# Kernel tuning notes

Measured on AMD Instinct MI355X. Metric: run time of the kernel, lower is better.

The kernel has to match this reference:

```python
import jax, jax.numpy as jnp
import numpy as np

N1 = 8192; N2 = 8192; E = 131072
D_IN = 128; H = 256; T = 32; B = 16
GCN_DIMS = [(D_IN, H), (H, H), (H, H)]


def _gcn_conv(x, edge_index, W):
    # PyG GCNConv (bias=False): add self-loops, symmetric D^-1/2 (A+I) D^-1/2 normalization.
    n = x.shape[0]
    h = x @ W
    loop = jnp.arange(n, dtype=edge_index.dtype)
    src = jnp.concatenate([edge_index[0], loop])
    dst = jnp.concatenate([edge_index[1], loop])
    deg = jax.ops.segment_sum(jnp.ones(dst.shape[0], h.dtype), dst, num_segments=n)
    dinv = jnp.where(deg > 0, jax.lax.rsqrt(deg), 0.0)
    norm = dinv[src] * dinv[dst]
    return jax.ops.segment_sum(norm[:, None] * h[src], dst, num_segments=n)


def _layer(f1, f2, ei1, ei2, Wg, Wu, bu, last):
    c1 = _gcn_conv(f1, ei1, Wg)
    c2 = _gcn_conv(f2, ei2, Wg)
    sim = f1 @ f2.T                      # [N1, N2] 'dot' similarity
    a1 = jax.nn.softmax(sim, axis=1)     # row softmax
    a2 = jax.nn.softmax(sim, axis=0)     # col softmax
    att1 = a1 @ f2                       # [N1, d]
    att2 = a2.T @ f1                     # [N2, d]
    g1 = jnp.concatenate([c1, f1, f1 - att1], axis=1) @ Wu + bu
    g2 = jnp.concatenate([c2, f2, f2 - att2], axis=1) @ Wu + bu
    if last:
        return g1, g2                    # last layer: no tanh, no dropout
    return jnp.tanh(g1), jnp.tanh(g2)    # dropout is a no-op in eval mode


def _forward(f1, f2, ei1, ei2, avg_v, gcn_Ws, upd_Ws, upd_bs,
             gated_W, gated_b, tn_W, tn_Wb, tn_b, fc1_W, fc1_b, sc_W, sc_b):
    n_layers = len(gcn_Ws)
    for i in range(n_layers):
        f1, f2 = _layer(f1, f2, ei1, ei2, gcn_Ws[i], upd_Ws[i], upd_bs[i],
                        last=(i == n_layers - 1))
    # gated readout: sum(sigmoid(gated(x)) * x)
    p1 = jnp.sum(jax.nn.sigmoid(f1 @ gated_W + gated_b) * f1, axis=0)  # [H]
    p2 = jnp.sum(jax.nn.sigmoid(f2 @ gated_W + gated_b) * f2, axis=0)  # [H]
    # NTN (TensorNetworkModule)
    scoring = jnp.einsum('i,ijt,j->t', p1, tn_W, p2)                   # bilinear term [T]
    block = tn_Wb @ jnp.concatenate([p1, p2])                          # [T]
    ntn = jax.nn.relu(scoring + block + tn_b)
    s = jnp.tanh(ntn @ fc1_W + fc1_b)                                  # [B]
    score = jax.nn.sigmoid(s @ sc_W + sc_b)                            # [1]
    pre_ged = -jnp.log(score) * avg_v                                  # target_mode='exp'
    return score.reshape(-1), pre_ged.reshape(-1)


def setup_inputs():
    key = jax.random.key(0)
    ks = jax.random.split(key, 32)
    rn = lambda k, sh, s=0.05: jax.random.normal(k, sh, dtype=jnp.float32) * s
    inp = {
        'features_1': jax.random.normal(ks[0], (N1, D_IN), dtype=jnp.float32),
        'features_2': jax.random.normal(ks[1], (N2, D_IN), dtype=jnp.float32),
        'edge_index_1': jax.random.randint(ks[2], (2, E), 0, N1, dtype=jnp.int32),
        'edge_index_2': jax.random.randint(ks[3], (2, E), 0, N2, dtype=jnp.int32),
        'avg_v': jnp.full((1,), 12.0, dtype=jnp.float32),
    }
    for i, (di, do) in enumerate(GCN_DIMS):
        inp[f'gcn_W{i}'] = rn(ks[4 + i], (di, do))
        inp[f'upd_W{i}'] = rn(ks[8 + i], (2 * di + do, do))
        inp[f'upd_b{i}'] = jnp.zeros((do,), jnp.float32)
    inp['gated_W'] = rn(ks[12], (H, H)); inp['gated_b'] = jnp.zeros((H,), jnp.float32)
    inp['tn_W'] = rn(ks[13], (H, H, T))
    inp['tn_Wb'] = rn(ks[14], (T, 2 * H)); inp['tn_b'] = jnp.zeros((T,), jnp.float32)
    inp['fc1_W'] = rn(ks[15], (T, B)); inp['fc1_b'] = jnp.zeros((B,), jnp.float32)
    inp['sc_W'] = rn(ks[16], (B, 1)); inp['sc_b'] = jnp.zeros((1,), jnp.float32)
    return inp


def reference(features_1, features_2, edge_index_1, edge_index_2, avg_v,
              gcn_W0, gcn_W1, gcn_W2, upd_W0, upd_W1, upd_W2,
              upd_b0, upd_b1, upd_b2, gated_W, gated_b,
              tn_W, tn_Wb, tn_b, fc1_W, fc1_b, sc_W, sc_b):
    return _forward(features_1, features_2, edge_index_1, edge_index_2, avg_v,
                    [gcn_W0, gcn_W1, gcn_W2], [upd_W0, upd_W1, upd_W2],
                    [upd_b0, upd_b1, upd_b2], gated_W, gated_b,
                    tn_W, tn_Wb, tn_b, fc1_W, fc1_b, sc_W, sc_b)
```

## Files before the change

kernel.cpp:

```cpp
#include <hip/hip_runtime.h>
#include <hip/hip_bf16.h>
#include <stdint.h>

#define NN 8192
#define EDG 131072
#define NSPLIT 4

typedef __attribute__((ext_vector_type(8))) short bf16x8;
typedef __attribute__((ext_vector_type(4))) float f32x4;
typedef unsigned short us;

__device__ __forceinline__ us f2bf(float f) {
  union { float f; unsigned u; } v; v.f = f;
  return (us)((v.u + 0x7fffu + ((v.u >> 16) & 1u)) >> 16);
}

__device__ __forceinline__ us f2bf_trunc(float f) {
  union { float f; unsigned u; } v; v.f = f;
  return (us)(v.u >> 16);
}

__device__ __forceinline__ float bf2f(us u) {
  union { unsigned u; float f; } v; v.u = ((unsigned)u) << 16;
  return v.f;
}

__device__ __forceinline__ void load_lds16(const void* g, void* l) {
  __builtin_amdgcn_global_load_lds(
      (__attribute__((address_space(1))) void*)(uintptr_t)g,
      (__attribute__((address_space(3))) void*)(uintptr_t)l,
      16, 0, 0);
}

template <int EPI>
__global__ __launch_bounds__(256) void gemm_k(
    const us* __restrict__ A, int lda, const us* __restrict__ Bt, int ldb,
    const float* __restrict__ bias, void* __restrict__ Cv, int ldc, int K) {
  __shared__ alignas(16) us As[64 * 32];
  __shared__ alignas(16) us Bs[128 * 32];
  const int t = threadIdx.x;
  const int wave = t >> 6, lane = t & 63;
  const int wrow = wave * 16;
  const int lrow = lane & 15, quad = lane >> 4;
  const int rowBase = blockIdx.x * 64;
  const int colBase = blockIdx.y * 128;
  const int sr = t >> 2, sch = t & 3;

  f32x4 acc[8];
#pragma unroll
  for (int j = 0; j < 8; j++) acc[j] = f32x4{0.f, 0.f, 0.f, 0.f};

  for (int kb = 0; kb < K; kb += 32) {
    __syncthreads();
    const us* asrc = A + (size_t)(rowBase + sr) * lda + kb + sch * 8;
    load_lds16(asrc, (char*)As + t * 16);
    const us* bsrc = Bt + (size_t)(colBase + sr) * ldb + kb + sch * 8;
    load_lds16(bsrc, (char*)Bs + t * 16);
    load_lds16(bsrc + (size_t)64 * ldb, (char*)Bs + t * 16 + 4096);
    __syncthreads();
    bf16x8 af = *(const bf16x8*)&As[(wrow + lrow) * 32 + quad * 8];
#pragma unroll
    for (int j = 0; j < 8; j++) {
      bf16x8 bfr = *(const bf16x8*)&Bs[(j * 16 + lrow) * 32 + quad * 8];
      acc[j] = __builtin_amdgcn_mfma_f32_16x16x32_bf16(af, bfr, acc[j], 0, 0, 0);
    }
  }

#pragma unroll
  for (int j = 0; j < 8; j++) {
    int col = colBase + j * 16 + lrow;
#pragma unroll
    for (int r = 0; r < 4; r++) {
      int row = rowBase + wrow + quad * 4 + r;
      size_t idx = (size_t)row * ldc + col;
      float v = acc[j][r];
      if (EPI == 0) ((float*)Cv)[idx] = v;
      else if (EPI == 2) ((float*)Cv)[idx] = v + bias[col];
      else if (EPI == 4) ((us*)Cv)[idx] = f2bf(v + bias[col]);
      else if (EPI == 5) ((us*)Cv)[idx] = f2bf(tanhf(v + bias[col]));
      else ((us*)Cv)[idx] = f2bf(v * bias[row]);
    }
  }
}

template <int DIN>
__global__ __launch_bounds__(256, 2) void flash_att(
    const us* __restrict__ Q, const us* __restrict__ K,
    const us* __restrict__ Vt, us* __restrict__ Opart,
    float* __restrict__ mpart, float* __restrict__ lpart, int kvPerSplit) {
  constexpr int NKC = DIN / 32;
  constexpr int OJ = DIN / 16;
  __shared__ alignas(16) us As[2][64 * 32];
  __shared__ alignas(16) us KB[2][256 * 32];
  __shared__ alignas(16) us Vs[2][DIN * 32];
  us* Ps = &KB[0][0];

  const int t = threadIdx.x;
  const int wave = t >> 6, lane = t & 63;
  const int wrow = wave * 16;
  const int lrow = lane & 15, quad = lane >> 4;
  const int rowBase = blockIdx.x * 64;
  const int split = blockIdx.y;
  const int kv0 = split * kvPerSplit;
  const int sr = t >> 2, sch = t & 3;
  const int pkey = ((lrow >> 2) ^ lrow) & 3;

  auto stageQ = [&](int kc, int buf) {
    const us* qsrc = Q + (size_t)(rowBase + sr) * DIN + kc * 32 + sch * 8;
    load_lds16(qsrc, (char*)&As[buf][0] + t * 16);
  };
  auto stageK = [&](int kt, int kc, int buf) {
    const us* ksrc = K + (size_t)(kt + sr) * DIN + kc * 32 + sch * 8;
#pragma unroll
    for (int p = 0; p < 4; p++)
      load_lds16(ksrc + (size_t)(p * 64) * DIN, (char*)&KB[buf][0] + p * 4096 + t * 16);
  };
  auto stageV = [&](int kt, int cc, int buf) {
#pragma unroll
    for (int p = 0; p < DIN / 64; p++) {
      const us* vsrc = Vt + (size_t)(p * 64 + sr) * NN + kt + cc * 32 + sch * 8;
      load_lds16(vsrc, (char*)&Vs[buf][0] + p * 4096 + t * 16);
    }
  };

  stageQ(0, 0);
  stageV(kv0, 0, 0);

  float m_i[4], l_i[4];
#pragma unroll
  for (int r = 0; r < 4; r++) { m_i[r] = -3.0e38f; l_i[r] = 0.f; }
  f32x4 accO[OJ];
#pragma unroll
  for (int j = 0; j < OJ; j++) accO[j] = f32x4{0.f, 0.f, 0.f, 0.f};

  for (int kt = kv0; kt < kv0 + kvPerSplit; kt += 256) {
    __syncthreads();
    stageK(kt, 0, 0);

    f32x4 accS[16];
#pragma unroll
    for (int j = 0; j < 16; j++) accS[j] = f32x4{0.f, 0.f, 0.f, 0.f};
    for (int kc = 0; kc < NKC; kc++) {
      const int buf = kc & 1;
      __syncthreads();
      if (kc + 1 < NKC) { stageK(kt, kc + 1, buf ^ 1); stageQ(kc + 1, buf ^ 1); }
      bf16x8 af = *(const bf16x8*)&As[buf][(wrow + lrow) * 32 + quad * 8];
#pragma unroll
      for (int j = 0; j < 16; j++) {
        bf16x8 bfr = *(const bf16x8*)&KB[buf][(j * 16 + lrow) * 32 + quad * 8];
        accS[j] = __builtin_amdgcn_mfma_f32_16x16x32_bf16(af, bfr, accS[j], 0, 0, 0);
      }
    }

    float alpha[4];
#pragma unroll
    for (int r = 0; r < 4; r++) {
      float v = accS[0][r];
#pragma unroll
      for (int j = 1; j < 16; j++) v = fmaxf(v, accS[j][r]);
#pragma unroll
      for (int mask = 1; mask < 16; mask <<= 1) v = fmaxf(v, __shfl_xor(v, mask));
      float mn = fmaxf(m_i[r], v);
      alpha[r] = __expf(m_i[r] - mn);
      m_i[r] = mn;
    }
    __syncthreads();
    float ts[4] = {0.f, 0.f, 0.f, 0.f};
#pragma unroll
    for (int j = 0; j < 16; j++)
#pragma unroll
      for (int r = 0; r < 4; r++) {
        float p = __expf(accS[j][r] - m_i[r]);
        ts[r] += p;
        int prow = wrow + quad * 4 + r;
        int key = (quad ^ r) & 3;
        int g = 2 * j + (lrow >> 3);
        Ps[prow * 256 + ((g ^ (key << 1)) << 3) + (lrow & 7)] = f2bf_trunc(p);
      }
#pragma unroll
    for (int r = 0; r < 4; r++) {
      float v = ts[r];
#pragma unroll
      for (int mask = 1; mask < 16; mask <<= 1) v += __shfl_xor(v, mask);
      l_i[r] = l_i[r] * alpha[r] + v;
    }
#pragma unroll
    for (int j = 0; j < OJ; j++)
#pragma unroll
      for (int r = 0; r < 4; r++) accO[j][r] *= alpha[r];

    const bool hasNext = (kt + 256 < kv0 + kvPerSplit);
    for (int cc = 0; cc < 8; cc++) {
      if (cc) __syncthreads();
      if (cc + 1 < 8) stageV(kt, cc + 1, (cc + 1) & 1);
      else if (hasNext) { stageV(kt + 256, 0, 0); stageQ(0, 0); }
      const int gk = cc * 4 + quad;
      bf16x8 af = *(const bf16x8*)&Ps[(wrow + lrow) * 256 + ((gk ^ (pkey << 1)) << 3)];
      const us* vb = &Vs[cc & 1][0];
#pragma unroll
      for (int j = 0; j < OJ; j++) {
        bf16x8 bfr = *(const bf16x8*)&vb[(j * 16 + lrow) * 32 + quad * 8];
        accO[j] = __builtin_amdgcn_mfma_f32_16x16x32_bf16(af, bfr, accO[j], 0, 0, 0);
      }
    }
  }

#pragma unroll
  for (int j = 0; j < OJ; j++)
#pragma unroll
    for (int r = 0; r < 4; r++) {
      int row = rowBase + wrow + quad * 4 + r;
      int col = j * 16 + lrow;
      Opart[((size_t)split * NN + row) * DIN + col] = f2bf(accO[j][r]);
    }
  if (lrow == 0) {
#pragma unroll
    for (int r = 0; r < 4; r++) {
      int row = rowBase + wrow + quad * 4 + r;
      mpart[(size_t)split * NN + row] = m_i[r];
      lpart[(size_t)split * NN + row] = l_i[r];
    }
  }
}

__global__ void merge_cat(const us* __restrict__ Op, const float* __restrict__ mp,
                          const float* __restrict__ lp, const us* __restrict__ cbuf,
                          const us* __restrict__ fbf, us* __restrict__ cat,
                          int din, int W) {
  int i = blockIdx.y;
  int c = blockIdx.x * 256 + threadIdx.x;
  us o;
  if (c < 256) {
    o = cbuf[(size_t)i * 256 + c];
  } else if (c < 256 + din) {
    o = fbf[(size_t)i * din + (c - 256)];
  } else {
    int f = c - 256 - din;
    float m[NSPLIT], w[NSPLIT];
    float M = -3.0e38f;
#pragma unroll
    for (int s = 0; s < NSPLIT; s++) { m[s] = mp[(size_t)s * NN + i]; M = fmaxf(M, m[s]); }
    float L = 0.f;
#pragma unroll
    for (int s = 0; s < NSPLIT; s++) { w[s] = __expf(m[s] - M); L += lp[(size_t)s * NN + i] * w[s]; }
    float a = 0.f;
#pragma unroll
    for (int s = 0; s < NSPLIT; s++)
      a += w[s] * bf2f(Op[((size_t)s * NN + i) * din + f]);
    o = f2bf(bf2f(fbf[(size_t)i * din + f]) - a / L);
  }
  cat[(size_t)i * W + c] = o;
}


__global__ void ws_sentinel(float* out) { out[0] = 12345.0f; out[1] = 12345.0f; }

__global__ void cvt_bf16(const float* __restrict__ in, us* __restrict__ out, int n) {
  int i = (blockIdx.x * 256 + threadIdx.x) * 4;
  if (i < n) {
    f32x4 v = *(const f32x4*)(in + i);
    uint2 p;
    p.x = f2bf(v.x) | ((unsigned)f2bf(v.y) << 16);
    p.y = f2bf(v.z) | ((unsigned)f2bf(v.w) << 16);
    *(uint2*)(out + i) = p;
  }
}

__global__ void transpose_bf16(const float* __restrict__ src, us* __restrict__ dst,
                               int R, int C) {
  __shared__ float tile[32][33];
  int c0 = blockIdx.x * 32, r0 = blockIdx.y * 32;
  int x = threadIdx.x, y = threadIdx.y;
  for (int i = y; i < 32; i += 8) tile[i][x] = src[(size_t)(r0 + i) * C + c0 + x];
  __syncthreads();
  for (int i = y; i < 32; i += 8) dst[(size_t)(c0 + i) * R + r0 + x] = f2bf(tile[x][i]);
}

__global__ void transpose_bb(const us* __restrict__ src, us* __restrict__ dst,
                             int R, int C) {
  __shared__ us tile[32][33];
  int c0 = blockIdx.x * 32, r0 = blockIdx.y * 32;
  int x = threadIdx.x, y = threadIdx.y;
  for (int i = y; i < 32; i += 8) tile[i][x] = src[(size_t)(r0 + i) * C + c0 + x];
  __syncthreads();
  for (int i = y; i < 32; i += 8) dst[(size_t)(c0 + i) * R + r0 + x] = tile[x][i];
}

__global__ void deg_count(const int* __restrict__ dst, int* __restrict__ deg) {
  int e = blockIdx.x * 256 + threadIdx.x;
  atomicAdd(&deg[dst[e]], 1);
}

__global__ void make_dinv(const int* __restrict__ deg, float* __restrict__ dinv) {
  int v = blockIdx.x * 256 + threadIdx.x;
  dinv[v] = rsqrtf((float)(deg[v] + 1));
}

__global__ void scan_deg(const int* __restrict__ deg, int* __restrict__ rowstart) {
  __shared__ int part[1024];
  int t = threadIdx.x;
  int base = t * 8;
  int local[8];
  int s = 0;
#pragma unroll
  for (int i = 0; i < 8; i++) { local[i] = s; s += deg[base + i]; }
  part[t] = s;
  __syncthreads();
  for (int off = 1; off < 1024; off <<= 1) {
    int v = (t >= off) ? part[t - off] : 0;
    __syncthreads();
    part[t] += v;
    __syncthreads();
  }
  int offset = (t == 0) ? 0 : part[t - 1];
#pragma unroll
  for (int i = 0; i < 8; i++) rowstart[base + i] = offset + local[i];
  if (t == 1023) rowstart[8192] = offset + s;
}

__global__ void csr_fill(const int* __restrict__ src, const int* __restrict__ dst,
                         int* __restrict__ cursor, int* __restrict__ csr_src) {
  int e = blockIdx.x * 256 + threadIdx.x;
  int pos = atomicAdd(&cursor[dst[e]], 1);
  csr_src[pos] = src[e];
}

__global__ __launch_bounds__(256) void gcn_agg_b(
    const int* __restrict__ rowstart, const int* __restrict__ csr_src,
    const float* __restrict__ dinv, const us* __restrict__ hs,
    us* __restrict__ c) {
  int node = blockIdx.x * 4 + (threadIdx.x >> 6);
  int lane = threadIdx.x & 63;
  const us* hp = hs + lane * 4;
  uint2 u = *(const uint2*)(hp + (size_t)node * 256);
  float a0 = bf2f(u.x & 0xffffu), a1 = bf2f(u.x >> 16);
  float a2 = bf2f(u.y & 0xffffu), a3 = bf2f(u.y >> 16);
  int s0 = rowstart[node], s1 = rowstart[node + 1];
  for (int j = s0; j < s1; j++) {
    int s = csr_src[j];
    uint2 v = *(const uint2*)(hp + (size_t)s * 256);
    a0 += bf2f(v.x & 0xffffu); a1 += bf2f(v.x >> 16);
    a2 += bf2f(v.y & 0xffffu); a3 += bf2f(v.y >> 16);
  }
  float dn = dinv[node];
  uint2 o;
  o.x = f2bf(a0 * dn) | ((unsigned)f2bf(a1 * dn) << 16);
  o.y = f2bf(a2 * dn) | ((unsigned)f2bf(a3 * dn) << 16);
  *(uint2*)(c + (size_t)node * 256 + lane * 4) = o;
}

__global__ void gated_pool(const float* __restrict__ q, const us* __restrict__ f,
                           float* __restrict__ p) {
  int col = threadIdx.x;
  int r0 = blockIdx.x * 128;
  float a = 0.f;
  for (int i = r0; i < r0 + 128; i++) {
    float qv = q[(size_t)i * 256 + col];
    a += bf2f(f[(size_t)i * 256 + col]) / (1.f + __expf(-qv));
  }
  atomicAdd(&p[col], a);
}

__global__ void ntn_bilinear(const float* __restrict__ p1, const float* __restrict__ tnW,
                             float* __restrict__ tmp) {
  int c = blockIdx.x * 256 + threadIdx.x;
  float a = 0.f;
#pragma unroll 8
  for (int i = 0; i < 256; i++) a += p1[i] * tnW[(size_t)i * 8192 + c];
  tmp[c] = a;
}

__global__ void ntn_final(const float* __restrict__ tmp, const float* __restrict__ p1,
                          const float* __restrict__ p2, const float* __restrict__ tnWb,
                          const float* __restrict__ tnb, const float* __restrict__ fc1W,
                          const float* __restrict__ fc1b, const float* __restrict__ scW,
                          const float* __restrict__ scb, const float* __restrict__ avgv,
                          float* __restrict__ out) {
  __shared__ float pc[512];
  __shared__ float ntn[32];
  __shared__ float sarr[16];
  int t = threadIdx.x;
  pc[t] = p1[t];
  pc[256 + t] = p2[t];
  __syncthreads();
  if (t < 32) {
    float sc = 0.f;
    for (int j = 0; j < 256; j++) sc += tmp[j * 32 + t] * pc[256 + j];
    float bl = 0.f;
    for (int k = 0; k < 512; k++) bl += tnWb[t * 512 + k] * pc[k];
    float v = sc + bl + tnb[t];
    ntn[t] = v > 0.f ? v : 0.f;
  }
  __syncthreads();
  if (t < 16) {
    float a = fc1b[t];
    for (int i = 0; i < 32; i++) a += ntn[i] * fc1W[i * 16 + t];
    sarr[t] = tanhf(a);
  }
  __syncthreads();
  if (t == 0) {
    float a = scb[0];
    for (int b = 0; b < 16; b++) a += sarr[b] * scW[b];
    float score = 1.f / (1.f + expf(-a));
    out[0] = score;
    out[1] = -logf(score) * avgv[0];
  }
}


extern "C" void kernel_launch(void* const* d_in, const int* in_sizes, int n_in,
                              void* d_out, int out_size, void* d_ws, size_t ws_size,
                              hipStream_t stream) {
  (void)in_sizes; (void)n_in; (void)out_size;
  const float* feat1 = (const float*)d_in[0];
  const float* feat2 = (const float*)d_in[1];
  const int* ei1 = (const int*)d_in[2];
  const int* ei2 = (const int*)d_in[3];
  const float* avgv = (const float*)d_in[4];
  const float* gcnW[3] = {(const float*)d_in[5], (const float*)d_in[8], (const float*)d_in[11]};
  const float* updW[3] = {(const float*)d_in[6], (const float*)d_in[9], (const float*)d_in[12]};
  const float* updb[3] = {(const float*)d_in[7], (const float*)d_in[10], (const float*)d_in[13]};
  const float* gatedW = (const float*)d_in[14];
  const float* gatedb = (const float*)d_in[15];
  const float* tnW = (const float*)d_in[16];
  const float* tnWb = (const float*)d_in[17];
  const float* tnb = (const float*)d_in[18];
  const float* fc1W = (const float*)d_in[19];
  const float* fc1b = (const float*)d_in[20];
  const float* scW = (const float*)d_in[21];
  const float* scb = (const float*)d_in[22];
  float* out = (float*)d_out;

  char* wp = (char*)d_ws;
  auto take = [&](size_t b) { char* p = wp; wp += (b + 255) & ~(size_t)255; return p; };
  us* Op = (us*)take((size_t)NSPLIT * NN * 256 * 2);
  us* cat1 = (us*)take((size_t)NN * 768 * 2);
  us* cat2 = (us*)take((size_t)NN * 768 * 2);
  us* fA1 = (us*)take((size_t)NN * 256 * 2);
  us* fA2 = (us*)take((size_t)NN * 256 * 2);
  us* fB1 = (us*)take((size_t)NN * 256 * 2);
  us* fB2 = (us*)take((size_t)NN * 256 * 2);
  us* f1bT = (us*)take((size_t)NN * 256 * 2);
  us* f2bT = (us*)take((size_t)NN * 256 * 2);
  us* hs1 = (us*)take((size_t)NN * 256 * 2);
  us* hs2 = (us*)take((size_t)NN * 256 * 2);
  us* cb1 = (us*)take((size_t)NN * 256 * 2);
  us* cb2 = (us*)take((size_t)NN * 256 * 2);
  float* q1 = (float*)take((size_t)NN * 256 * 4);
  float* q2 = (float*)take((size_t)NN * 256 * 4);
  us* WgT[3], *WuT[3];
  for (int l = 0; l < 3; l++) WgT[l] = (us*)take(256 * 256 * 2);
  for (int l = 0; l < 3; l++) WuT[l] = (us*)take(256 * 768 * 2);
  us* gWT = (us*)take(256 * 256 * 2);
  int* deg1 = (int*)take(NN * 4);
  int* deg2 = (int*)take(NN * 4);
  float* dinv1 = (float*)take(NN * 4);
  float* dinv2 = (float*)take(NN * 4);
  int* rs1 = (int*)take((NN + 1) * 4);
  int* rs2 = (int*)take((NN + 1) * 4);
  int* cur1 = (int*)take(NN * 4);
  int* cur2 = (int*)take(NN * 4);
  int* csr1 = (int*)take((size_t)EDG * 4);
  int* csr2 = (int*)take((size_t)EDG * 4);
  float* mp = (float*)take((size_t)NSPLIT * NN * 4);
  float* lp = (float*)take((size_t)NSPLIT * NN * 4);
  float* p1 = (float*)take(1024);
  float* p2 = (float*)take(1024);
  float* tmp = (float*)take(NN * 4);

  size_t need = (size_t)(wp - (char*)d_ws);
  if (need > ws_size) {
    ws_sentinel<<<1, 1, 0, stream>>>(out);
    return;
  }

  hipMemsetAsync(deg1, 0, NN * 4, stream);
  hipMemsetAsync(deg2, 0, NN * 4, stream);
  deg_count<<<EDG / 256, 256, 0, stream>>>(ei1 + EDG, deg1);
  deg_count<<<EDG / 256, 256, 0, stream>>>(ei2 + EDG, deg2);
  make_dinv<<<NN / 256, 256, 0, stream>>>(deg1, dinv1);
  make_dinv<<<NN / 256, 256, 0, stream>>>(deg2, dinv2);
  scan_deg<<<1, 1024, 0, stream>>>(deg1, rs1);
  scan_deg<<<1, 1024, 0, stream>>>(deg2, rs2);
  hipMemcpyAsync(cur1, rs1, NN * 4, hipMemcpyDeviceToDevice, stream);
  hipMemcpyAsync(cur2, rs2, NN * 4, hipMemcpyDeviceToDevice, stream);
  csr_fill<<<EDG / 256, 256, 0, stream>>>(ei1, ei1 + EDG, cur1, csr1);
  csr_fill<<<EDG / 256, 256, 0, stream>>>(ei2, ei2 + EDG, cur2, csr2);

  for (int l = 0; l < 3; l++) {
    int din = (l == 0) ? 128 : 256;
    int W = 256 + 2 * din;
    transpose_bf16<<<dim3(8, din / 32), dim3(32, 8), 0, stream>>>(gcnW[l], WgT[l], din, 256);
    transpose_bf16<<<dim3(8, W / 32), dim3(32, 8), 0, stream>>>(updW[l], WuT[l], W, 256);
  }
  transpose_bf16<<<dim3(8, 8), dim3(32, 8), 0, stream>>>(gatedW, gWT, 256, 256);

  us* f1 = fA1; us* f2 = fA2;
  us* fn1 = fB1; us* fn2 = fB2;
  cvt_bf16<<<NN * 128 / 1024, 256, 0, stream>>>(feat1, f1, NN * 128);
  cvt_bf16<<<NN * 128 / 1024, 256, 0, stream>>>(feat2, f2, NN * 128);

  for (int l = 0; l < 3; l++) {
    const int din = (l == 0) ? 128 : 256;
    const int W = 256 + 2 * din;

    if (l == 0) {
      transpose_bf16<<<dim3(din / 32, NN / 32), dim3(32, 8), 0, stream>>>(feat1, f1bT, NN, din);
      transpose_bf16<<<dim3(din / 32, NN / 32), dim3(32, 8), 0, stream>>>(feat2, f2bT, NN, din);
    } else {
      transpose_bb<<<dim3(din / 32, NN / 32), dim3(32, 8), 0, stream>>>(f1, f1bT, NN, din);
      transpose_bb<<<dim3(din / 32, NN / 32), dim3(32, 8), 0, stream>>>(f2, f2bT, NN, din);
    }

    gemm_k<6><<<dim3(128, 2), 256, 0, stream>>>(f1, din, WgT[l], din, dinv1, hs1, 256, din);
    gemm_k<6><<<dim3(128, 2), 256, 0, stream>>>(f2, din, WgT[l], din, dinv2, hs2, 256, din);

    gcn_agg_b<<<NN / 4, 256, 0, stream>>>(rs1, csr1, dinv1, hs1, cb1);
    gcn_agg_b<<<NN / 4, 256, 0, stream>>>(rs2, csr2, dinv2, hs2, cb2);

    if (l == 0) {
      flash_att<128><<<dim3(NN / 64, NSPLIT), 256, 0, stream>>>(f1, f2, f2bT, Op, mp, lp, NN / NSPLIT);
      merge_cat<<<dim3(W / 256, NN), 256, 0, stream>>>(Op, mp, lp, cb1, f1, cat1, din, W);
      flash_att<128><<<dim3(NN / 64, NSPLIT), 256, 0, stream>>>(f2, f1, f1bT, Op, mp, lp, NN / NSPLIT);
      merge_cat<<<dim3(W / 256, NN), 256, 0, stream>>>(Op, mp, lp, cb2, f2, cat2, din, W);
    } else {
      flash_att<256><<<dim3(NN / 64, NSPLIT), 256, 0, stream>>>(f1, f2, f2bT, Op, mp, lp, NN / NSPLIT);
      merge_cat<<<dim3(W / 256, NN), 256, 0, stream>>>(Op, mp, lp, cb1, f1, cat1, din, W);
      flash_att<256><<<dim3(NN / 64, NSPLIT), 256, 0, stream>>>(f2, f1, f1bT, Op, mp, lp, NN / NSPLIT);
      merge_cat<<<dim3(W / 256, NN), 256, 0, stream>>>(Op, mp, lp, cb2, f2, cat2, din, W);
    }

    if (l < 2) {
      gemm_k<5><<<dim3(128, 2), 256, 0, stream>>>(cat1, W, WuT[l], W, updb[l], fn1, 256, W);
      gemm_k<5><<<dim3(128, 2), 256, 0, stream>>>(cat2, W, WuT[l], W, updb[l], fn2, 256, W);
    } else {
      gemm_k<4><<<dim3(128, 2), 256, 0, stream>>>(cat1, W, WuT[l], W, updb[l], fn1, 256, W);
      gemm_k<4><<<dim3(128, 2), 256, 0, stream>>>(cat2, W, WuT[l], W, updb[l], fn2, 256, W);
    }
    us* s;
    s = f1; f1 = fn1; fn1 = s;
    s = f2; f2 = fn2; fn2 = s;
  }

  gemm_k<2><<<dim3(128, 2), 256, 0, stream>>>(f1, 256, gWT, 256, gatedb, q1, 256, 256);
  gemm_k<2><<<dim3(128, 2), 256, 0, stream>>>(f2, 256, gWT, 256, gatedb, q2, 256, 256);
  hipMemsetAsync(p1, 0, 256 * 4, stream);
  hipMemsetAsync(p2, 0, 256 * 4, stream);
  gated_pool<<<64, 256, 0, stream>>>(q1, f1, p1);
  gated_pool<<<64, 256, 0, stream>>>(q2, f2, p2);

  ntn_bilinear<<<32, 256, 0, stream>>>(p1, tnW, tmp);
  ntn_final<<<1, 256, 0, stream>>>(tmp, p1, p2, tnWb, tnb, fc1W, fc1b, scW, scb, avgv, out);
}
```

Baseline: 1.216 ms.

## Use 2x2 wave tiling in flash attention with cross-wave softmax reduction

Reassigns the four waves of the flash attention block from a 4x1 row split to a 2x2 tile split. Each wave now computes 32 rows by half the key columns for QK^T and half the output columns for PV. This lets each B-fragment LDS read feed two MFMAs, cutting LDS traffic per MFMA. In exchange, row max and row sum must be combined across wave pairs through shared memory, which adds an extra barrier and small LDS arrays per KV tile.

Measured after the change: 1.412 ms. +16.1%, slower.

```diff
diff --git a/kernel.cpp b/kernel.cpp
--- a/kernel.cpp
+++ b/kernel.cpp
@@ -89,15 +89,18 @@
     const us* __restrict__ Vt, us* __restrict__ Opart,
     float* __restrict__ mpart, float* __restrict__ lpart, int kvPerSplit) {
   constexpr int NKC = DIN / 32;
-  constexpr int OJ = DIN / 16;
+  constexpr int OJ = DIN / 32;
   __shared__ alignas(16) us As[2][64 * 32];
   __shared__ alignas(16) us KB[2][256 * 32];
   __shared__ alignas(16) us Vs[2][DIN * 32];
+  __shared__ float redM[2][64];
+  __shared__ float redL[2][64];
   us* Ps = &KB[0][0];
 
   const int t = threadIdx.x;
   const int wave = t >> 6, lane = t & 63;
-  const int wrow = wave * 16;
+  const int wr = wave >> 1;
+  const int wc = wave & 1;
   const int lrow = lane & 15, quad = lane >> 4;
   const int rowBase = blockIdx.x * 64;
   const int split = blockIdx.y;
@@ -126,68 +129,115 @@
   stageQ(0, 0);
   stageV(kv0, 0, 0);
 
-  float m_i[4], l_i[4];
-#pragma unroll
-  for (int r = 0; r < 4; r++) { m_i[r] = -3.0e38f; l_i[r] = 0.f; }
-  f32x4 accO[OJ];
-#pragma unroll
-  for (int j = 0; j < OJ; j++) accO[j] = f32x4{0.f, 0.f, 0.f, 0.f};
+  float m_i[8], l_i[8];
+#pragma unroll
+  for (int x = 0; x < 8; x++) { m_i[x] = -3.0e38f; l_i[x] = 0.f; }
+  f32x4 accO[2][OJ];
+#pragma unroll
+  for (int i = 0; i < 2; i++)
+#pragma unroll
+    for (int j = 0; j < OJ; j++) accO[i][j] = f32x4{0.f, 0.f, 0.f, 0.f};
 
   for (int kt = kv0; kt < kv0 + kvPerSplit; kt += 256) {
     __syncthreads();
     stageK(kt, 0, 0);
 
-    f32x4 accS[16];
-#pragma unroll
-    for (int j = 0; j < 16; j++) accS[j] = f32x4{0.f, 0.f, 0.f, 0.f};
+    f32x4 accS[2][8];
+#pragma unroll
+    for (int i = 0; i < 2; i++)
+#pragma unroll
+      for (int j = 0; j < 8; j++) accS[i][j] = f32x4{0.f, 0.f, 0.f, 0.f};
     for (int kc = 0; kc < NKC; kc++) {
       const int buf = kc & 1;
       __syncthreads();
       if (kc + 1 < NKC) { stageK(kt, kc + 1, buf ^ 1); stageQ(kc + 1, buf ^ 1); }
-      bf16x8 af = *(const bf16x8*)&As[buf][(wrow + lrow) * 32 + quad * 8];
-#pragma unroll
-      for (int j = 0; j < 16; j++) {
-        bf16x8 bfr = *(const bf16x8*)&KB[buf][(j * 16 + lrow) * 32 + quad * 8];
-        accS[j] = __builtin_amdgcn_mfma_f32_16x16x32_bf16(af, bfr, accS[j], 0, 0, 0);
+      bf16x8 af[2];
+#pragma unroll
+      for (int i = 0; i < 2; i++)
+        af[i] = *(const bf16x8*)&As[buf][(wr * 32 + i * 16 + lrow) * 32 + quad * 8];
+#pragma unroll
+      for (int j = 0; j < 8; j++) {
+        bf16x8 bfr = *(const bf16x8*)&KB[buf][(wc * 128 + j * 16 + lrow) * 32 + quad * 8];
+#pragma unroll
+        for (int i = 0; i < 2; i++)
+          accS[i][j] = __builtin_amdgcn_mfma_f32_16x16x32_bf16(af[i], bfr, accS[i][j], 0, 0, 0);
       }
     }
 
-    float alpha[4];
-#pragma unroll
-    for (int r = 0; r < 4; r++) {
-      float v = accS[0][r];
-#pragma unroll
-      for (int j = 1; j < 16; j++) v = fmaxf(v, accS[j][r]);
-#pragma unroll
-      for (int mask = 1; mask < 16; mask <<= 1) v = fmaxf(v, __shfl_xor(v, mask));
-      float mn = fmaxf(m_i[r], v);
-      alpha[r] = __expf(m_i[r] - mn);
-      m_i[r] = mn;
+    float tm[8];
+#pragma unroll
+    for (int i = 0; i < 2; i++)
+#pragma unroll
+      for (int r = 0; r < 4; r++) {
+        float v = accS[i][0][r];
+#pragma unroll
+        for (int j = 1; j < 8; j++) v = fmaxf(v, accS[i][j][r]);
+#pragma unroll
+        for (int mask = 1; mask < 16; mask <<= 1) v = fmaxf(v, __shfl_xor(v, mask));
+        tm[i * 4 + r] = v;
+      }
+    if (lrow == 0) {
+#pragma unroll
+      for (int i = 0; i < 2; i++)
+#pragma unroll
+        for (int r = 0; r < 4; r++)
+          redM[wc][wr * 32 + i * 16 + quad * 4 + r] = tm[i * 4 + r];
     }
     __syncthreads();
-    float ts[4] = {0.f, 0.f, 0.f, 0.f};
-#pragma unroll
-    for (int j = 0; j < 16; j++)
+    float alpha[8];
+#pragma unroll
+    for (int i = 0; i < 2; i++)
 #pragma unroll
       for (int r = 0; r < 4; r++) {
-        float p = __expf(accS[j][r] - m_i[r]);
-        ts[r] += p;
-        int prow = wrow + quad * 4 + r;
-        int key = (quad ^ r) & 3;
-        int g = 2 * j + (lrow >> 3);
-        Ps[prow * 256 + ((g ^ (key << 1)) << 3) + (lrow & 7)] = f2bf_trunc(p);
+        int x = i * 4 + r, row = wr * 32 + i * 16 + quad * 4 + r;
+        float mt = fmaxf(redM[0][row], redM[1][row]);
+        float mn = fmaxf(m_i[x], mt);
+        alpha[x] = __expf(m_i[x] - mn);
+        m_i[x] = mn;
       }
-#pragma unroll
-    for (int r = 0; r < 4; r++) {
-      float v = ts[r];
-#pragma unroll
-      for (int mask = 1; mask < 16; mask <<= 1) v += __shfl_xor(v, mask);
-      l_i[r] = l_i[r] * alpha[r] + v;
-    }
-#pragma unroll
-    for (int j = 0; j < OJ; j++)
-#pragma unroll
-      for (int r = 0; r < 4; r++) accO[j][r] *= alpha[r];
+    float ts[8];
+#pragma unroll
+    for (int x = 0; x < 8; x++) ts[x] = 0.f;
+#pragma unroll
+    for (int i = 0; i < 2; i++)
+#pragma unroll
+      for (int j = 0; j < 8; j++)
+#pragma unroll
+        for (int r = 0; r < 4; r++) {
+          int x = i * 4 + r;
+          float p = __expf(accS[i][j][r] - m_i[x]);
+          ts[x] += p;
+          int prow = wr * 32 + i * 16 + quad * 4 + r;
+          int key = (quad ^ r) & 3;
+          int g = 2 * (wc * 8 + j) + (lrow >> 3);
+          Ps[prow * 256 + ((g ^ (key << 1)) << 3) + (lrow & 7)] = f2bf_trunc(p);
+        }
+#pragma unroll
+    for (int x = 0; x < 8; x++) {
+#pragma unroll
+      for (int mask = 1; mask < 16; mask <<= 1) ts[x] += __shfl_xor(ts[x], mask);
+    }
+    if (lrow == 0) {
+#pragma unroll
+      for (int i = 0; i < 2; i++)
+#pragma unroll
+        for (int r = 0; r < 4; r++)
+          redL[wc][wr * 32 + i * 16 + quad * 4 + r] = ts[i * 4 + r];
+    }
+#pragma unroll
+    for (int i = 0; i < 2; i++)
+#pragma unroll
+      for (int j = 0; j < OJ; j++)
+#pragma unroll
+        for (int r = 0; r < 4; r++) accO[i][j][r] *= alpha[i * 4 + r];
+    __syncthreads();
+#pragma unroll
+    for (int i = 0; i < 2; i++)
+#pragma unroll
+      for (int r = 0; r < 4; r++) {
+        int x = i * 4 + r, row = wr * 32 + i * 16 + quad * 4 + r;
+        l_i[x] = l_i[x] * alpha[x] + redL[0][row] + redL[1][row];
+      }
 
     const bool hasNext = (kt + 256 < kv0 + kvPerSplit);
     for (int cc = 0; cc < 8; cc++) {
@@ -195,31 +245,40 @@
       if (cc + 1 < 8) stageV(kt, cc + 1, (cc + 1) & 1);
       else if (hasNext) { stageV(kt + 256, 0, 0); stageQ(0, 0); }
       const int gk = cc * 4 + quad;
-      bf16x8 af = *(const bf16x8*)&Ps[(wrow + lrow) * 256 + ((gk ^ (pkey << 1)) << 3)];
+      bf16x8 af[2];
+#pragma unroll
+      for (int i = 0; i < 2; i++)
+        af[i] = *(const bf16x8*)&Ps[(wr * 32 + i * 16 + lrow) * 256 + ((gk ^ (pkey << 1)) << 3)];
       const us* vb = &Vs[cc & 1][0];
 #pragma unroll
       for (int j = 0; j < OJ; j++) {
-        bf16x8 bfr = *(const bf16x8*)&vb[(j * 16 + lrow) * 32 + quad * 8];
-        accO[j] = __builtin_amdgcn_mfma_f32_16x16x32_bf16(af, bfr, accO[j], 0, 0, 0);
+        bf16x8 bfr = *(const bf16x8*)&vb[(wc * (DIN / 2) + j * 16 + lrow) * 32 + quad * 8];
+#pragma unroll
+        for (int i = 0; i < 2; i++)
+          accO[i][j] = __builtin_amdgcn_mfma_f32_16x16x32_bf16(af[i], bfr, accO[i][j], 0, 0, 0);
       }
     }
   }
 
 #pragma unroll
-  for (int j = 0; j < OJ; j++)
-#pragma unroll
-    for (int r = 0; r < 4; r++) {
-      int row = rowBase + wrow + quad * 4 + r;
-      int col = j * 16 + lrow;
-      Opart[((size_t)split * NN + row) * DIN + col] = f2bf(accO[j][r]);
-    }
-  if (lrow == 0) {
-#pragma unroll
-    for (int r = 0; r < 4; r++) {
-      int row = rowBase + wrow + quad * 4 + r;
-      mpart[(size_t)split * NN + row] = m_i[r];
-      lpart[(size_t)split * NN + row] = l_i[r];
-    }
+  for (int i = 0; i < 2; i++)
+#pragma unroll
+    for (int j = 0; j < OJ; j++)
+#pragma unroll
+      for (int r = 0; r < 4; r++) {
+        int row = rowBase + wr * 32 + i * 16 + quad * 4 + r;
+        int col = wc * (DIN / 2) + j * 16 + lrow;
+        Opart[((size_t)split * NN + row) * DIN + col] = f2bf(accO[i][j][r]);
+      }
+  if (lrow == 0 && wc == 0) {
+#pragma unroll
+    for (int i = 0; i < 2; i++)
+#pragma unroll
+      for (int r = 0; r < 4; r++) {
+        int row = rowBase + wr * 32 + i * 16 + quad * 4 + r;
+        mpart[(size_t)split * NN + row] = m_i[i * 4 + r];
+        lpart[(size_t)split * NN + row] = l_i[i * 4 + r];
+      }
   }
 }
 
```
